# Optimization experiments

Hardware: AMD Instinct MI355X
Metric: run time of the kernel (lower is better)

## Reference

```python
import jax, jax.numpy as jnp
import numpy as np

BATCH, N_DIM, N_CLASS = 32, 512, 100
BIG_NEG = 1000000.0


def _get_upper_box(z, w, b):
    # z: (B, 2, n_dim) box domain; w: (B, n_dim, S, S); b: (B, S, S)
    z_min, z_max = z[:, 0], z[:, 1]
    center = 0.5 * (z_min + z_max)      # (B, n_dim)
    radius = 0.5 * (z_max - z_min)      # (B, n_dim)
    lin = jnp.einsum('bn,bnij->bij', center, w)
    amp = jnp.einsum('bn,bnij->bij', radius, jnp.abs(w))
    return b + lin + amp


def setup_inputs() -> dict:
    key = jax.random.key(0)
    ks = jax.random.split(key, 8)
    x = jax.random.normal(ks[0], (BATCH, N_DIM), dtype=jnp.float32)
    # box domain: lower <= upper
    lower = jax.random.normal(ks[1], (BATCH, N_DIM), dtype=jnp.float32)
    width = jax.random.uniform(ks[2], (BATCH, N_DIM), dtype=jnp.float32) * 0.1
    z_tensor = jnp.stack([lower, lower + width], axis=1)  # (B, 2, n_dim)
    w_u = jax.random.normal(ks[3], (BATCH, N_DIM, N_CLASS), dtype=jnp.float32) * 0.05
    b_u = jax.random.normal(ks[4], (BATCH, N_CLASS), dtype=jnp.float32)
    w_l = jax.random.normal(ks[5], (BATCH, N_DIM, N_CLASS), dtype=jnp.float32) * 0.05
    b_l = jax.random.normal(ks[6], (BATCH, N_CLASS), dtype=jnp.float32)
    labels = jax.random.randint(ks[7], (BATCH,), 0, N_CLASS)
    y_tensor = jax.nn.one_hot(labels, N_CLASS, dtype=jnp.float32)
    return {"x": x, "z_tensor": z_tensor, "w_u": w_u, "b_u": b_u,
            "w_l": w_l, "b_l": b_l, "y_tensor": y_tensor}


def reference(x, z_tensor, w_u, b_u, w_l, b_l, y_tensor):
    # ibp=False, forward=True, mode='forward' -> adv_score = get_forward_score(...)
    source = y_tensor                 # (B, S), one-hot
    target = 1.0 - source             # (B, S)
    # broadcasted outer difference: (B, n_dim, S_target, S_source)
    w_f = w_u[:, :, :, None] - w_l[:, :, None, :]
    b_f = (b_u[:, :, None] - b_l[:, None, :]
           - BIG_NEG * (1.0 - source)[:, None, :]
           - BIG_NEG * (1.0 - target)[:, :, None])
    upper = _get_upper_box(z_tensor, w_f, b_f)  # (B, S, S)
    return jnp.max(upper, axis=(-1, -2))        # (B,)
```

## Files before the change

### kernel.cpp

```cpp
#include <hip/hip_runtime.h>
#include <math.h>
#include <stdint.h>

#define BATCH 32
#define ND 512
#define NC 100
#define BIGNEG 1000000.0f

__device__ __forceinline__ float rdlane_f(float v, int t) {
  return __uint_as_float(__builtin_amdgcn_readlane(__float_as_uint(v), (uint32_t)t));
}

__global__ __launch_bounds__(1024, 2) void adv_one(
    const float* __restrict__ z, const float* __restrict__ wu,
    const float* __restrict__ bu, const float* __restrict__ wl,
    const float* __restrict__ bl, const float* __restrict__ y,
    float* __restrict__ out)
{
  const int b   = blockIdx.x;
  const int tid = threadIdx.x;
  const int wv  = tid >> 6, l = tid & 63;
  const int pair = wv >> 1, half = wv & 1;

  __shared__ int   s_js;
  __shared__ float s_dq[8];
  __shared__ float s_amp[8][128];
  __shared__ float s_dot[8][128];
  __shared__ float s_mx[16];

  if (tid == 0) s_js = 0;
  __syncthreads();
  if (tid < NC && y[b * NC + tid] > 0.5f) s_js = tid;
  __syncthreads();
  const int js = s_js;

  const int n = (pair << 6) + l;
  const float* zb = z + (size_t)b * 2 * ND;
  const float zlo = zb[n], zhi = zb[ND + n];
  const float cc = zlo + zhi;
  const float rr = zhi - zlo;
  const float qv = wl[((size_t)b * ND + n) * NC + js];

  if (half == 0) {
    float p = cc * qv;
#pragma unroll
    for (int off = 1; off < 64; off <<= 1) p += __shfl_xor(p, off, 64);
    if (l == 0) s_dq[pair] = p;
  }

  const int i  = (half << 6) + l;
  const int iL = (i < NC) ? i : NC - 1;
  const float* up = wu + ((size_t)b * ND + (pair << 6)) * NC + iL;

  float amp = 0.f, dotu = 0.f;
#pragma unroll 8
  for (int t = 0; t < 64; ++t) {
    float u  = up[(size_t)t * NC];
    float cs = rdlane_f(cc, t);
    float rs = rdlane_f(rr, t);
    float qs = rdlane_f(qv, t);
    float d  = u - qs;
    amp  = fmaf(rs, fabsf(d), amp);
    dotu = fmaf(cs, u, dotu);
  }
  s_amp[pair][tid & 127] = amp;
  s_dot[pair][tid & 127] = dotu;
  __syncthreads();

  float m = -INFINITY;
  if (tid < NC) {
    float A = 0.f, Du = 0.f, dq = 0.f;
#pragma unroll
    for (int p = 0; p < 8; ++p) {
      A += s_amp[p][tid]; Du += s_dot[p][tid]; dq += s_dq[p];
    }
    m = bu[b * NC + tid] - BIGNEG * y[b * NC + tid] - bl[b * NC + js]
        + 0.5f * (Du - dq + A);
  }
#pragma unroll
  for (int off = 32; off; off >>= 1) m = fmaxf(m, __shfl_down(m, off, 64));
  if (l == 0) s_mx[wv] = m;
  __syncthreads();
  if (tid == 0) {
    float r = s_mx[0];
#pragma unroll
    for (int k = 1; k < 16; ++k) r = fmaxf(r, s_mx[k]);
    out[b] = r;
  }
}

extern "C" void kernel_launch(void* const* d_in, const int* in_sizes, int n_in,
                              void* d_out, int out_size, void* d_ws, size_t ws_size,
                              hipStream_t stream) {
  const float* z  = (const float*)d_in[1];
  const float* wu = (const float*)d_in[2];
  const float* bu = (const float*)d_in[3];
  const float* wl = (const float*)d_in[4];
  const float* bl = (const float*)d_in[5];
  const float* y  = (const float*)d_in[6];

  adv_one<<<BATCH, 1024, 0, stream>>>(z, wu, bu, wl, bl, y, (float*)d_out);
}
```

Baseline: 12.19 us.

## Split per-batch kernel into 256 partial blocks plus a finalize kernel

Replaces the single 32-block, 1024-thread kernel with a two-kernel scheme. The first kernel spreads each batch's 512-dim reduction over 8 small 128-thread blocks (256 blocks in total, block ids remapped) and writes partial sums to workspace. A second small kernel combines the partials and takes the max. The aim is to use more CUs and fetch the weights with more parallelism, at the cost of an extra launch and a global round trip for the partials. The unroll factor also goes from 8 to 16.

```diff
diff --git a/kernel.cpp b/kernel.cpp
--- a/kernel.cpp
+++ b/kernel.cpp
@@ -5,28 +5,25 @@
 #define BATCH 32
 #define ND 512
 #define NC 100
+#define NQ 8
 #define BIGNEG 1000000.0f
 
 __device__ __forceinline__ float rdlane_f(float v, int t) {
   return __uint_as_float(__builtin_amdgcn_readlane(__float_as_uint(v), (uint32_t)t));
 }
 
-__global__ __launch_bounds__(1024, 2) void adv_one(
+__global__ __launch_bounds__(128, 8) void adv_part(
     const float* __restrict__ z, const float* __restrict__ wu,
-    const float* __restrict__ bu, const float* __restrict__ wl,
-    const float* __restrict__ bl, const float* __restrict__ y,
-    float* __restrict__ out)
+    const float* __restrict__ wl, const float* __restrict__ y,
+    float* __restrict__ P)
 {
-  const int b   = blockIdx.x;
-  const int tid = threadIdx.x;
-  const int wv  = tid >> 6, l = tid & 63;
-  const int pair = wv >> 1, half = wv & 1;
+  const int id = ((blockIdx.x & 7) << 5) + (blockIdx.x >> 3);
+  const int b = id >> 3, nq = id & 7;
+  const int tid  = threadIdx.x;
+  const int half = tid >> 6, l = tid & 63;
 
   __shared__ int   s_js;
-  __shared__ float s_dq[8];
-  __shared__ float s_amp[8][128];
-  __shared__ float s_dot[8][128];
-  __shared__ float s_mx[16];
+  __shared__ float s_dq;
 
   if (tid == 0) s_js = 0;
   __syncthreads();
@@ -34,7 +31,8 @@
   __syncthreads();
   const int js = s_js;
 
-  const int n = (pair << 6) + l;
+  const int n0 = nq << 6;
+  const int n  = n0 + l;
   const float* zb = z + (size_t)b * 2 * ND;
   const float zlo = zb[n], zhi = zb[ND + n];
   const float cc = zlo + zhi;
@@ -45,15 +43,15 @@
     float p = cc * qv;
 #pragma unroll
     for (int off = 1; off < 64; off <<= 1) p += __shfl_xor(p, off, 64);
-    if (l == 0) s_dq[pair] = p;
+    if (l == 0) s_dq = p;
   }
 
   const int i  = (half << 6) + l;
   const int iL = (i < NC) ? i : NC - 1;
-  const float* up = wu + ((size_t)b * ND + (pair << 6)) * NC + iL;
+  const float* up = wu + ((size_t)b * ND + n0) * NC + iL;
 
   float amp = 0.f, dotu = 0.f;
-#pragma unroll 8
+#pragma unroll 16
   for (int t = 0; t < 64; ++t) {
     float u  = up[(size_t)t * NC];
     float cs = rdlane_f(cc, t);
@@ -63,30 +61,38 @@
     amp  = fmaf(rs, fabsf(d), amp);
     dotu = fmaf(cs, u, dotu);
   }
-  s_amp[pair][tid & 127] = amp;
-  s_dot[pair][tid & 127] = dotu;
   __syncthreads();
+  P[(size_t)id * 128 + tid] = amp + dotu - s_dq;
+}
+
+__global__ __launch_bounds__(128) void adv_fin(
+    const float* __restrict__ P, const float* __restrict__ bu,
+    const float* __restrict__ bl, const float* __restrict__ y,
+    float* __restrict__ out)
+{
+  const int b = blockIdx.x, tid = threadIdx.x;
+  __shared__ int   s_js;
+  __shared__ float s_mx[2];
+
+  if (tid == 0) s_js = 0;
+  __syncthreads();
+  if (tid < NC && y[b * NC + tid] > 0.5f) s_js = tid;
+  __syncthreads();
+  const int js = s_js;
 
   float m = -INFINITY;
   if (tid < NC) {
-    float A = 0.f, Du = 0.f, dq = 0.f;
+    const float* pb = P + ((size_t)b * NQ) * 128 + tid;
+    float s = 0.f;
 #pragma unroll
-    for (int p = 0; p < 8; ++p) {
-      A += s_amp[p][tid]; Du += s_dot[p][tid]; dq += s_dq[p];
-    }
-    m = bu[b * NC + tid] - BIGNEG * y[b * NC + tid] - bl[b * NC + js]
-        + 0.5f * (Du - dq + A);
+    for (int q = 0; q < NQ; ++q) s += pb[q * 128];
+    m = bu[b * NC + tid] - BIGNEG * y[b * NC + tid] - bl[b * NC + js] + 0.5f * s;
   }
 #pragma unroll
   for (int off = 32; off; off >>= 1) m = fmaxf(m, __shfl_down(m, off, 64));
-  if (l == 0) s_mx[wv] = m;
+  if ((tid & 63) == 0) s_mx[tid >> 6] = m;
   __syncthreads();
-  if (tid == 0) {
-    float r = s_mx[0];
-#pragma unroll
-    for (int k = 1; k < 16; ++k) r = fmaxf(r, s_mx[k]);
-    out[b] = r;
-  }
+  if (tid == 0) out[b] = fmaxf(s_mx[0], s_mx[1]);
 }
 
 extern "C" void kernel_launch(void* const* d_in, const int* in_sizes, int n_in,
@@ -98,6 +104,8 @@
   const float* wl = (const float*)d_in[4];
   const float* bl = (const float*)d_in[5];
   const float* y  = (const float*)d_in[6];
+  float* P = (float*)d_ws;
 
-  adv_one<<<BATCH, 1024, 0, stream>>>(z, wu, bu, wl, bl, y, (float*)d_out);
+  adv_part<<<BATCH * NQ, 128, 0, stream>>>(z, wu, wl, y, P);
+  adv_fin<<<BATCH, 128, 0, stream>>>(P, bu, bl, y, (float*)d_out);
 }
```

After: 11.77 us (median of 2 runs). 3.4% less time.
